# Kernel tuning notes

Measured on AMD Instinct MI355X. Metric: run time of the kernel, lower is better.

## Reference

```python
import jax, jax.numpy as jnp
import numpy as np
import math

B, S, D = 2, 2048, 2048
HQ, HKV = 16, 4            # query heads, kv heads
HD = D // HQ               # head dim = 128
REPS = HQ // HKV           # queries per kv head = 4
KVD = HKV * HD             # 512


def setup_inputs() -> dict:
    key = jax.random.key(0)
    ks = jax.random.split(key, 7)
    s = 0.02
    return {
        "hidden_states": jax.random.normal(ks[0], (B, S, D), dtype=jnp.float32),
        "Wq": jax.random.normal(ks[1], (D, D), dtype=jnp.float32) * s,
        "bq": jnp.zeros((D,), dtype=jnp.float32),
        "Wk": jax.random.normal(ks[2], (D, KVD), dtype=jnp.float32) * s,
        "bk": jnp.zeros((KVD,), dtype=jnp.float32),
        "Wv": jax.random.normal(ks[3], (D, KVD), dtype=jnp.float32) * s,
        "bv": jnp.zeros((KVD,), dtype=jnp.float32),
    }


def reference(hidden_states, Wq, bq, Wk, bk, Wv, bv):
    b, s, d = hidden_states.shape
    # Projections
    q = hidden_states @ Wq + bq                      # [B,S,D]
    k = hidden_states @ Wk + bk                      # [B,S,KVD]
    v = hidden_states @ Wv + bv                      # [B,S,KVD]
    # Split heads. torch repeat_kv_heads uses .repeat (tile), so expanded
    # head h maps to kv head (h mod HKV). Reshape q heads as (REPS, HKV)
    # so axis g indexes the kv head, matching that tiling exactly.
    q = q.reshape(b, s, HQ, HD).transpose(0, 2, 1, 3)          # [B,HQ,S,hd]
    q = q.reshape(b, REPS, HKV, s, HD)                          # [B,R,G,S,hd]
    k = k.reshape(b, s, HKV, HD).transpose(0, 2, 1, 3)          # [B,G,S,hd]
    v = v.reshape(b, s, HKV, HD).transpose(0, 2, 1, 3)          # [B,G,S,hd]
    scale = 1.0 / math.sqrt(HD)
    scores = jnp.einsum('brgsd,bgtd->brgst', q, k) * scale      # [B,R,G,S,S]
    probs = jax.nn.softmax(scores, axis=-1)
    ctx = jnp.einsum('brgst,bgtd->brgsd', probs, v)             # [B,R,G,S,hd]
    ctx = ctx.reshape(b, HQ, s, HD).transpose(0, 2, 1, 3)       # [B,S,HQ,hd]
    return ctx.reshape(b, s, HQ * HD)                            # [B,S,D]
```

## Files before the change

kernel.cpp:

```cpp
#include <hip/hip_runtime.h>
#include <hip/hip_bf16.h>

#define QSCALE   0.08838834764831845f
#define QKSCALE  0.1275174468755322f

typedef __attribute__((ext_vector_type(8))) short bh8;
typedef __attribute__((ext_vector_type(4))) float fx4;
typedef __attribute__((ext_vector_type(4))) short sh4;

typedef const __attribute__((address_space(1))) unsigned GAu;
typedef __attribute__((address_space(3))) unsigned LAu;

__device__ __forceinline__ short f2bf(float f) {
    unsigned u = __float_as_uint(f);
    unsigned r = u + 0x7fffu + ((u >> 16) & 1u);
    return (short)(r >> 16);
}

__device__ __forceinline__ unsigned pk_bf16(float x, float y) {
    union { __hip_bfloat162 h; unsigned u; } cv;
    cv.h = __float22bfloat162_rn(float2{x, y});
    return cv.u;
}

__global__ __launch_bounds__(256) void prep_all(
    const float* __restrict__ x,  short* __restrict__ xo,
    const float* __restrict__ wq, short* __restrict__ wqt,
    const float* __restrict__ wk, short* __restrict__ wkt,
    const float* __restrict__ wv, short* __restrict__ wvt) {
    __shared__ float tile[64][65];
    const int bid = blockIdx.x;
    const int tid = threadIdx.x;

    if (bid < 8192) {
        int i = bid * 256 + tid;
        float4 v = ((const float4*)x)[i];
        sh4 s;
        s.x = f2bf(v.x); s.y = f2bf(v.y); s.z = f2bf(v.z); s.w = f2bf(v.w);
        ((sh4*)xo)[i] = s;
        return;
    }

    const float* w; short* wt; int N, nb, kb;
    int t = bid - 8192;
    if (t < 1024)      { w = wq; wt = wqt; N = 2048; nb = t & 31; kb = t >> 5; }
    else if (t < 1280) { w = wk; wt = wkt; N = 512;  t -= 1024; nb = t & 7; kb = t >> 3; }
    else               { w = wv; wt = wvt; N = 512;  t -= 1280; nb = t & 7; kb = t >> 3; }
    const int K = 2048;

    {
        int c4 = tid & 15, r0 = tid >> 4;
#pragma unroll
        for (int rr = 0; rr < 4; ++rr) {
            int r = r0 + rr * 16;
            float4 v = *(const float4*)&w[(size_t)(kb * 64 + r) * N + nb * 64 + c4 * 4];
            *(float4*)&tile[r][c4 * 4] = v;
        }
    }
    __syncthreads();
    {
        int k4 = tid & 15, n0 = tid >> 4;
#pragma unroll
        for (int rr = 0; rr < 4; ++rr) {
            int n = n0 + rr * 16;
            sh4 s;
            s.x = f2bf(tile[k4 * 4 + 0][n]);
            s.y = f2bf(tile[k4 * 4 + 1][n]);
            s.z = f2bf(tile[k4 * 4 + 2][n]);
            s.w = f2bf(tile[k4 * 4 + 3][n]);
            *(sh4*)&wt[(size_t)(nb * 64 + n) * K + kb * 64 + k4 * 4] = s;
        }
    }
}

__global__ __launch_bounds__(256) void proj_gemm(
    const short* __restrict__ X,
    const short* __restrict__ WqT,
    const short* __restrict__ WkT,
    const short* __restrict__ WvT,
    const float* __restrict__ bq, const float* __restrict__ bk,
    const float* __restrict__ bv,
    short* __restrict__ Qb, short* __restrict__ Kpk, short* __restrict__ Vpk) {
    __shared__ short As0[128 * 32];
    __shared__ short As1[128 * 32];
    __shared__ short Bs0[128 * 32];
    __shared__ short Bs1[128 * 32];

    const int tid = threadIdx.x;
    const int bm = blockIdx.x;
    const int ntg = blockIdx.y;

    const short* Wm; const float* bias; int col0, kind;
    if (ntg < 16)      { Wm = WqT; bias = bq; col0 = ntg * 128;        kind = 0; }
    else if (ntg < 20) { Wm = WkT; bias = bk; col0 = (ntg - 16) * 128; kind = 1; }
    else               { Wm = WvT; bias = bv; col0 = (ntg - 20) * 128; kind = 2; }

    const int w = tid >> 6, lane = tid & 63, quad = lane >> 4, l16 = lane & 15;

    fx4 acc[2][8];
#pragma unroll
    for (int i = 0; i < 2; ++i)
#pragma unroll
        for (int j = 0; j < 8; ++j) acc[i][j] = fx4{0.f, 0.f, 0.f, 0.f};

    const int srow = w * 16 + (lane >> 2);
    const int scol = (((lane & 3) ^ ((lane >> 2) & 3)) * 8);
    const short* Ag = X + (size_t)(bm * 128 + srow) * 2048 + scol;
    const short* Bg = Wm + (size_t)(col0 + srow) * 2048 + scol;
    const int stoff = w * 512;

    const int fchunk = (quad ^ (l16 & 3)) * 8;
    const int aoff0 = (w * 32 + l16) * 32 + fchunk;
    const int aoff1 = aoff0 + 512;
    const int boff  = l16 * 32 + fchunk;

    const short* pA00 = As0 + aoff0;  const short* pA01 = As0 + aoff1;
    const short* pA10 = As1 + aoff0;  const short* pA11 = As1 + aoff1;
    const short* pB0  = Bs0 + boff;   const short* pB1  = Bs1 + boff;

#define PG_STAGE(AsD, BsD, ktile)                                               \
    do {                                                                        \
        const int k0_ = (ktile) * 32;                                           \
        _Pragma("unroll")                                                       \
        for (int j = 0; j < 2; ++j) {                                           \
            __builtin_amdgcn_global_load_lds(                                   \
                (GAu*)(Ag + (size_t)(j * 64) * 2048 + k0_),                     \
                (LAu*)(AsD + stoff + j * 2048), 16, 0, 0);                      \
            __builtin_amdgcn_global_load_lds(                                   \
                (GAu*)(Bg + (size_t)(j * 64) * 2048 + k0_),                     \
                (LAu*)(BsD + stoff + j * 2048), 16, 0, 0);                      \
        }                                                                       \
    } while (0)

#define PG_COMPUTE(pA0_, pA1_, pB_)                                             \
    do {                                                                        \
        bh8 af0 = *(const bh8*)(pA0_);                                          \
        bh8 af1 = *(const bh8*)(pA1_);                                          \
        _Pragma("unroll")                                                       \
        for (int nt = 0; nt < 8; ++nt) {                                        \
            bh8 bf = *(const bh8*)((pB_) + nt * 512);                           \
            acc[0][nt] = __builtin_amdgcn_mfma_f32_16x16x32_bf16(af0, bf, acc[0][nt], 0, 0, 0); \
            acc[1][nt] = __builtin_amdgcn_mfma_f32_16x16x32_bf16(af1, bf, acc[1][nt], 0, 0, 0); \
        }                                                                       \
    } while (0)

    PG_STAGE(As0, Bs0, 0);
    __syncthreads();

    for (int kt = 0; kt < 64; kt += 2) {
        PG_STAGE(As1, Bs1, kt + 1);
        PG_COMPUTE(pA00, pA01, pB0);
        __syncthreads();

        if (kt < 62) PG_STAGE(As0, Bs0, kt + 2);
        PG_COMPUTE(pA10, pA11, pB1);
        __syncthreads();
    }
#undef PG_STAGE
#undef PG_COMPUTE

#pragma unroll
    for (int mt = 0; mt < 2; ++mt) {
        int srow2 = bm * 128 + w * 32 + mt * 16 + quad * 4;
#pragma unroll
        for (int nt = 0; nt < 8; ++nt) {
            int c = col0 + nt * 16 + l16;
            float bval = bias[c];
#pragma unroll
            for (int r = 0; r < 4; ++r) {
                int sg = srow2 + r;
                int b = sg >> 11, s = sg & 2047;
                float v = acc[mt][nt][r] + bval;
                int hd = c & 127;
                if (kind == 0) {
                    v *= QKSCALE;
                    int h = c >> 7;
                    Qb[(((size_t)(b * 16 + h) * 2048 + s) << 7) + hd] = f2bf(v);
                } else if (kind == 1) {
                    int g = c >> 7;
                    int kt32 = s >> 5, u = s & 31;
                    int nti = (u >> 2) & 1, fl16 = (u >> 3) * 4 + (u & 3);
                    int ks = hd >> 5, qd = (hd >> 3) & 3, j = hd & 7;
                    size_t frag = (((size_t)(b * 4 + g) * 64 + kt32) * 8 + nti * 4 + ks);
                    Kpk[frag * 512 + (qd * 16 + fl16) * 8 + j] = f2bf(v);
                } else {
                    int g = c >> 7;
                    int ktt = s >> 6, tl = s & 63;
                    int ts = tl >> 5, qd = (tl >> 3) & 3, j = tl & 7;
                    int fnt = hd >> 4, fl16 = hd & 15;
                    size_t frag = (((size_t)(b * 4 + g) * 32 + ktt) * 16 + fnt * 2 + ts);
                    Vpk[frag * 512 + (qd * 16 + fl16) * 8 + j] = f2bf(v);
                }
            }
        }
    }
}

__global__ __launch_bounds__(128, 2) void attn(
    const short* __restrict__ Qb,
    const short* __restrict__ Kpk,
    const short* __restrict__ Vpk,
    float* __restrict__ out) {
    __shared__ short Ks0[8 * 512];
    __shared__ short Ks1[8 * 512];
    __shared__ short Vs0[8 * 512];
    __shared__ short Vs1[8 * 512];

    const int bid = blockIdx.x;
    const int gb = bid & 7;
    const int rep = (bid >> 3) & 3;
    const int qt = bid >> 5;
    const int b = gb >> 2, g = gb & 3;
    const int h = rep * 4 + g;
    const int tid = threadIdx.x, w = tid >> 6, lane = tid & 63;
    const int quad = lane >> 4, l16 = lane & 15;

    bh8 qf[2][4];
#pragma unroll
    for (int rg = 0; rg < 2; ++rg) {
        int s = qt * 64 + w * 32 + rg * 16 + l16;
        const short* qp = Qb + (((size_t)(b * 16 + h) * 2048 + s) << 7);
#pragma unroll
        for (int ks = 0; ks < 4; ++ks)
            qf[rg][ks] = *(const bh8*)(qp + ks * 32 + quad * 8);
    }

    const short* kbase = Kpk + ((size_t)gb * 32) * 8192;
    const short* vbase = Vpk + ((size_t)gb * 32) * 8192;

    const short* pK0 = Ks0 + lane * 8;
    const short* pK1 = Ks1 + lane * 8;
    const short* pV0 = Vs0 + lane * 8;
    const short* pV1 = Vs1 + lane * 8;

    fx4 ctx[2][8];
#pragma unroll
    for (int rg = 0; rg < 2; ++rg)
#pragma unroll
        for (int j = 0; j < 8; ++j) ctx[rg][j] = fx4{0.f, 0.f, 0.f, 0.f};
    float l_part[2] = {0.f, 0.f};

    const bh8 z8 = bh8{0, 0, 0, 0, 0, 0, 0, 0};
    bh8 paP[2] = {z8, z8};
    bh8 vfA[8], vfB[8];
#pragma unroll
    for (int f = 0; f < 8; ++f) { vfA[f] = z8; vfB[f] = z8; }

#define AT_BARRIER()  asm volatile("s_waitcnt lgkmcnt(0)\n\ts_barrier" ::: "memory")
#define AT_VM(N)      asm volatile("s_waitcnt vmcnt(" #N ")" ::: "memory")

#define AT_STAGE(KsD, VsD, kn)                                                  \
    do {                                                                        \
        const short* kp_ = kbase + (size_t)(kn) * 4096;                         \
        const short* vp_ = vbase + (size_t)((kn) >> 1) * 8192 + ((kn) & 1) * 512;\
        _Pragma("unroll")                                                       \
        for (int i = 0; i < 4; ++i) {                                           \
            int f = w * 4 + i;                                                  \
            __builtin_amdgcn_global_load_lds((GAu*)(kp_ + f * 512 + lane * 8),  \
                                             (LAu*)(KsD + f * 512), 16, 0, 0);  \
            __builtin_amdgcn_global_load_lds((GAu*)(vp_ + (size_t)f * 1024 + lane * 8),\
                                             (LAu*)(VsD + f * 512), 16, 0, 0);  \
        }                                                                       \
    } while (0)

#define AT_COMPUTE(pKC, pVC, vfC, vfP)                                          \
    do {                                                                        \
        _Pragma("unroll")                                                       \
        for (int nt = 0; nt < 8; ++nt)                                          \
            vfC[nt] = *(const bh8*)((pVC) + nt * 512);                          \
        fx4 sc[2][2];                                                           \
        sc[0][0] = fx4{0.f, 0.f, 0.f, 0.f}; sc[0][1] = fx4{0.f, 0.f, 0.f, 0.f}; \
        sc[1][0] = fx4{0.f, 0.f, 0.f, 0.f}; sc[1][1] = fx4{0.f, 0.f, 0.f, 0.f}; \
        __builtin_amdgcn_s_setprio(1);                                          \
        _Pragma("unroll")                                                       \
        for (int nti = 0; nti < 2; ++nti) {                                     \
            _Pragma("unroll")                                                   \
            for (int ks = 0; ks < 4; ++ks) {                                    \
                bh8 kf = *(const bh8*)((pKC) + (nti * 4 + ks) * 512);           \
                sc[0][nti] = __builtin_amdgcn_mfma_f32_16x16x32_bf16(kf, qf[0][ks], sc[0][nti], 0, 0, 0); \
                sc[1][nti] = __builtin_amdgcn_mfma_f32_16x16x32_bf16(kf, qf[1][ks], sc[1][nti], 0, 0, 0); \
            }                                                                   \
        }                                                                       \
        _Pragma("unroll")                                                       \
        for (int nt = 0; nt < 8; ++nt) {                                        \
            ctx[0][nt] = __builtin_amdgcn_mfma_f32_16x16x32_bf16(paP[0], vfP[nt], ctx[0][nt], 0, 0, 0); \
            ctx[1][nt] = __builtin_amdgcn_mfma_f32_16x16x32_bf16(paP[1], vfP[nt], ctx[1][nt], 0, 0, 0); \
        }                                                                       \
        __builtin_amdgcn_s_setprio(0);                                          \
        _Pragma("unroll")                                                       \
        for (int rg = 0; rg < 2; ++rg) {                                        \
            float e0 = __builtin_amdgcn_exp2f(sc[rg][0][0]);                    \
            float e1 = __builtin_amdgcn_exp2f(sc[rg][0][1]);                    \
            float e2 = __builtin_amdgcn_exp2f(sc[rg][0][2]);                    \
            float e3 = __builtin_amdgcn_exp2f(sc[rg][0][3]);                    \
            float e4 = __builtin_amdgcn_exp2f(sc[rg][1][0]);                    \
            float e5 = __builtin_amdgcn_exp2f(sc[rg][1][1]);                    \
            float e6 = __builtin_amdgcn_exp2f(sc[rg][1][2]);                    \
            float e7 = __builtin_amdgcn_exp2f(sc[rg][1][3]);                    \
            l_part[rg] += ((e0 + e1) + (e2 + e3)) + ((e4 + e5) + (e6 + e7));    \
            unsigned a[4];                                                      \
            a[0] = pk_bf16(e0, e1);                                             \
            a[1] = pk_bf16(e2, e3);                                             \
            a[2] = pk_bf16(e4, e5);                                             \
            a[3] = pk_bf16(e6, e7);                                             \
            paP[rg] = *(const bh8*)a;                                           \
        }                                                                       \
    } while (0)

    AT_STAGE(Ks0, Vs0, 0);
    AT_STAGE(Ks1, Vs1, 1);
    AT_VM(0);
    AT_BARRIER();

    for (int kt = 0; kt < 62; kt += 2) {
        AT_COMPUTE(pK0, pV0, vfA, vfB);
        AT_BARRIER();
        AT_STAGE(Ks0, Vs0, kt + 2);
        AT_VM(8);
        AT_BARRIER();
        AT_COMPUTE(pK1, pV1, vfB, vfA);
        AT_BARRIER();
        AT_STAGE(Ks1, Vs1, kt + 3);
        AT_VM(8);
        AT_BARRIER();
    }
    AT_COMPUTE(pK0, pV0, vfA, vfB);
    AT_VM(0);
    AT_BARRIER();
    AT_COMPUTE(pK1, pV1, vfB, vfA);
#pragma unroll
    for (int nt = 0; nt < 8; ++nt) {
        ctx[0][nt] = __builtin_amdgcn_mfma_f32_16x16x32_bf16(paP[0], vfB[nt], ctx[0][nt], 0, 0, 0);
        ctx[1][nt] = __builtin_amdgcn_mfma_f32_16x16x32_bf16(paP[1], vfB[nt], ctx[1][nt], 0, 0, 0);
    }
#undef AT_STAGE
#undef AT_COMPUTE
#undef AT_BARRIER
#undef AT_VM

#pragma unroll
    for (int rg = 0; rg < 2; ++rg) {
        float lsum = l_part[rg];
        lsum += __shfl_xor(lsum, 16);
        lsum += __shfl_xor(lsum, 32);
        int srow = qt * 64 + w * 32 + rg * 16 + quad * 4;
#pragma unroll
        for (int r = 0; r < 4; ++r) {
            float inv = 1.f / __shfl(lsum, quad * 4 + r);
            size_t rowoff = ((size_t)b * 2048 + (srow + r)) * 2048 + h * 128;
#pragma unroll
            for (int nt = 0; nt < 8; ++nt)
                out[rowoff + nt * 16 + l16] = ctx[rg][nt][r] * inv;
        }
    }
}

extern "C" void kernel_launch(void* const* d_in, const int* in_sizes, int n_in,
                              void* d_out, int out_size, void* d_ws, size_t ws_size,
                              hipStream_t stream) {
    const float* hs = (const float*)d_in[0];
    const float* Wq = (const float*)d_in[1];
    const float* bq = (const float*)d_in[2];
    const float* Wk = (const float*)d_in[3];
    const float* bk = (const float*)d_in[4];
    const float* Wv = (const float*)d_in[5];
    const float* bv = (const float*)d_in[6];
    float* out = (float*)d_out;

    char* ws = (char*)d_ws;
    short* Xbf = (short*)(ws);
    short* WqT = (short*)(ws + 16777216);
    short* WkT = (short*)(ws + 25165824);
    short* WvT = (short*)(ws + 27262976);
    short* Qb  = (short*)(ws + 29360128);
    short* Kpk = (short*)(ws + 46137344);
    short* Vpk = (short*)(ws + 50331648);

    prep_all<<<9728, 256, 0, stream>>>(hs, Xbf, Wq, WqT, Wk, WkT, Wv, WvT);
    proj_gemm<<<dim3(32, 24), 256, 0, stream>>>(Xbf, WqT, WkT, WvT, bq, bk, bv,
                                                Qb, Kpk, Vpk);
    attn<<<1024, 128, 0, stream>>>(Qb, Kpk, Vpk, out);
}
```

Baseline: 258.0 us.

## Load projection GEMM A operand directly from global, stage only weights in LDS

The projection GEMM now reads each wave's A fragments (activation rows) directly from global memory into registers instead of staging them through shared memory, since each wave owns distinct rows. Only the weight tile is double-buffered in LDS, with a doubled K step of 64 per stage, halving barrier count. Launch bounds request 3 blocks per CU. This removes LDS traffic and staging for A, but exposes global load latency on the MFMA path without prefetch and uses less coalesced strided row reads.

```diff
diff --git a/kernel.cpp b/kernel.cpp
--- a/kernel.cpp
+++ b/kernel.cpp
@@ -73,7 +73,7 @@
     }
 }
 
-__global__ __launch_bounds__(256) void proj_gemm(
+__global__ __launch_bounds__(256, 3) void proj_gemm(
     const short* __restrict__ X,
     const short* __restrict__ WqT,
     const short* __restrict__ WkT,
@@ -81,10 +81,8 @@
     const float* __restrict__ bq, const float* __restrict__ bk,
     const float* __restrict__ bv,
     short* __restrict__ Qb, short* __restrict__ Kpk, short* __restrict__ Vpk) {
-    __shared__ short As0[128 * 32];
-    __shared__ short As1[128 * 32];
-    __shared__ short Bs0[128 * 32];
-    __shared__ short Bs1[128 * 32];
+    __shared__ short Bs0[2 * 128 * 32];
+    __shared__ short Bs1[2 * 128 * 32];
 
     const int tid = threadIdx.x;
     const int bm = blockIdx.x;
@@ -105,55 +103,63 @@
 
     const int srow = w * 16 + (lane >> 2);
     const int scol = (((lane & 3) ^ ((lane >> 2) & 3)) * 8);
-    const short* Ag = X + (size_t)(bm * 128 + srow) * 2048 + scol;
     const short* Bg = Wm + (size_t)(col0 + srow) * 2048 + scol;
     const int stoff = w * 512;
 
+    const short* Ap = X + (size_t)(bm * 128 + w * 32 + l16) * 2048 + quad * 8;
+
     const int fchunk = (quad ^ (l16 & 3)) * 8;
-    const int aoff0 = (w * 32 + l16) * 32 + fchunk;
-    const int aoff1 = aoff0 + 512;
     const int boff  = l16 * 32 + fchunk;
-
-    const short* pA00 = As0 + aoff0;  const short* pA01 = As0 + aoff1;
-    const short* pA10 = As1 + aoff0;  const short* pA11 = As1 + aoff1;
-    const short* pB0  = Bs0 + boff;   const short* pB1  = Bs1 + boff;
-
-#define PG_STAGE(AsD, BsD, ktile)                                               \
+    const short* pB00 = Bs0 + boff;
+    const short* pB01 = Bs0 + 4096 + boff;
+    const short* pB10 = Bs1 + boff;
+    const short* pB11 = Bs1 + 4096 + boff;
+
+#define PG_STAGE(BsD, ktile)                                                    \
     do {                                                                        \
-        const int k0_ = (ktile) * 32;                                           \
-        _Pragma("unroll")                                                       \
-        for (int j = 0; j < 2; ++j) {                                           \
-            __builtin_amdgcn_global_load_lds(                                   \
-                (GAu*)(Ag + (size_t)(j * 64) * 2048 + k0_),                     \
-                (LAu*)(AsD + stoff + j * 2048), 16, 0, 0);                      \
-            __builtin_amdgcn_global_load_lds(                                   \
-                (GAu*)(Bg + (size_t)(j * 64) * 2048 + k0_),                     \
-                (LAu*)(BsD + stoff + j * 2048), 16, 0, 0);                      \
+        _Pragma("unroll")                                                       \
+        for (int ks = 0; ks < 2; ++ks) {                                        \
+            const int k0_ = (ktile) * 64 + ks * 32;                             \
+            _Pragma("unroll")                                                   \
+            for (int j = 0; j < 2; ++j) {                                       \
+                __builtin_amdgcn_global_load_lds(                               \
+                    (GAu*)(Bg + (size_t)(j * 64) * 2048 + k0_),                 \
+                    (LAu*)(BsD + ks * 4096 + stoff + j * 2048), 16, 0, 0);      \
+            }                                                                   \
         }                                                                       \
     } while (0)
 
-#define PG_COMPUTE(pA0_, pA1_, pB_)                                             \
+#define PG_COMPUTE(pBk0, pBk1, ktile)                                           \
     do {                                                                        \
-        bh8 af0 = *(const bh8*)(pA0_);                                          \
-        bh8 af1 = *(const bh8*)(pA1_);                                          \
+        const size_t ko_ = (size_t)(ktile) * 64;                                \
+        bh8 a00 = *(const bh8*)(Ap + ko_);                                      \
+        bh8 a10 = *(const bh8*)(Ap + 32768 + ko_);                              \
+        bh8 a01 = *(const bh8*)(Ap + ko_ + 32);                                 \
+        bh8 a11 = *(const bh8*)(Ap + 32768 + ko_ + 32);                         \
         _Pragma("unroll")                                                       \
         for (int nt = 0; nt < 8; ++nt) {                                        \
-            bh8 bf = *(const bh8*)((pB_) + nt * 512);                           \
-            acc[0][nt] = __builtin_amdgcn_mfma_f32_16x16x32_bf16(af0, bf, acc[0][nt], 0, 0, 0); \
-            acc[1][nt] = __builtin_amdgcn_mfma_f32_16x16x32_bf16(af1, bf, acc[1][nt], 0, 0, 0); \
+            bh8 bf = *(const bh8*)((pBk0) + nt * 512);                          \
+            acc[0][nt] = __builtin_amdgcn_mfma_f32_16x16x32_bf16(a00, bf, acc[0][nt], 0, 0, 0); \
+            acc[1][nt] = __builtin_amdgcn_mfma_f32_16x16x32_bf16(a10, bf, acc[1][nt], 0, 0, 0); \
+        }                                                                       \
+        _Pragma("unroll")                                                       \
+        for (int nt = 0; nt < 8; ++nt) {                                        \
+            bh8 bf = *(const bh8*)((pBk1) + nt * 512);                          \
+            acc[0][nt] = __builtin_amdgcn_mfma_f32_16x16x32_bf16(a01, bf, acc[0][nt], 0, 0, 0); \
+            acc[1][nt] = __builtin_amdgcn_mfma_f32_16x16x32_bf16(a11, bf, acc[1][nt], 0, 0, 0); \
         }                                                                       \
     } while (0)
 
-    PG_STAGE(As0, Bs0, 0);
+    PG_STAGE(Bs0, 0);
     __syncthreads();
 
-    for (int kt = 0; kt < 64; kt += 2) {
-        PG_STAGE(As1, Bs1, kt + 1);
-        PG_COMPUTE(pA00, pA01, pB0);
+    for (int kt = 0; kt < 32; kt += 2) {
+        PG_STAGE(Bs1, kt + 1);
+        PG_COMPUTE(pB00, pB01, kt);
         __syncthreads();
 
-        if (kt < 62) PG_STAGE(As0, Bs0, kt + 2);
-        PG_COMPUTE(pA10, pA11, pB1);
+        if (kt < 30) PG_STAGE(Bs0, kt + 2);
+        PG_COMPUTE(pB10, pB11, kt + 1);
         __syncthreads();
     }
 #undef PG_STAGE
```

Result: faster. 249.6 us (-3.3%).
